# Optimization experiments

Hardware: AMD Instinct MI355X
Metric: run time of the kernel (lower is better)

The kernel has to match this reference:

```python
import jax, jax.numpy as jnp
import numpy as np

H = 256
B = 4096          # number of graphs / motifs in batch
NF = 131072       # focal atoms
NR = 262144       # residues
V = 8001          # vocab.size() + 1
TOPK = 5
DIST_THRESH = 6.0


def setup_inputs() -> dict:
    key = jax.random.key(0)
    ks = jax.random.split(key, 12)
    h_ctx_focal = jax.random.normal(ks[0], (NF, H), dtype=jnp.float32)
    pos_ctx_focal = jax.random.normal(ks[1], (NF, 3), dtype=jnp.float32)
    current_wid = jax.random.randint(ks[2], (B,), 0, V)
    current_atoms_batch = jnp.sort(jax.random.randint(ks[3], (NF,), 0, B))
    h_residue = jax.random.normal(ks[4], (NR, H), dtype=jnp.float32)
    residue_pos = jax.random.normal(ks[5], (NR, 3, 3), dtype=jnp.float32)
    amino_acid_batch = jnp.sort(jax.random.randint(ks[6], (NR,), 0, B))
    emb_weight = jax.random.normal(ks[7], (V, H), dtype=jnp.float32) * 0.02
    mlp_w1 = jax.random.normal(ks[8], (3 * H, H), dtype=jnp.float32) * (1.0 / np.sqrt(3 * H))
    mlp_b1 = jnp.zeros((H,), dtype=jnp.float32)
    mlp_w2 = jax.random.normal(ks[9], (H, H), dtype=jnp.float32) * (1.0 / np.sqrt(H))
    mlp_b2 = jnp.zeros((H,), dtype=jnp.float32)
    return {
        'h_ctx_focal': h_ctx_focal, 'pos_ctx_focal': pos_ctx_focal,
        'current_wid': current_wid, 'current_atoms_batch': current_atoms_batch,
        'h_residue': h_residue, 'residue_pos': residue_pos,
        'amino_acid_batch': amino_acid_batch, 'emb_weight': emb_weight,
        'mlp_w1': mlp_w1, 'mlp_b1': mlp_b1, 'mlp_w2': mlp_w2, 'mlp_b2': mlp_b2,
    }


def reference(h_ctx_focal, pos_ctx_focal, current_wid, current_atoms_batch,
              h_residue, residue_pos, amino_acid_batch,
              emb_weight, mlp_w1, mlp_b1, mlp_w2, mlp_b2):
    nB = current_wid.shape[0]
    # scatter_add over focal atoms -> [B, H]
    node_hiddens = jax.ops.segment_sum(h_ctx_focal, current_atoms_batch, num_segments=nB)
    # embedding lookup -> [B, H]
    motif_hiddens = emb_weight[current_wid]
    # scatter_mean of positions -> [B, 3]
    pos_sum = jax.ops.segment_sum(pos_ctx_focal, current_atoms_batch, num_segments=nB)
    counts = jax.ops.segment_sum(jnp.ones((pos_ctx_focal.shape[0],), jnp.float32),
                                 current_atoms_batch, num_segments=nB)
    center_pos = pos_sum / jnp.maximum(counts, 1.0)[:, None]
    # CA position of each residue, distance mask (< 6 A from motif center)
    ca_pos = residue_pos[:, 1, :]                                  # [NR, 3]
    dist = jnp.linalg.norm(ca_pos - center_pos[amino_acid_batch], axis=1)
    mask = dist < DIST_THRESH                                      # [NR]
    # masked scatter_add of residue embeddings -> [B, H]
    residue_emb = jax.ops.segment_sum(jnp.where(mask[:, None], h_residue, 0.0),
                                      amino_acid_batch, num_segments=nB)
    # motif MLP (2 layers) + projection onto embedding table
    pred_vecs = jnp.concatenate([node_hiddens, motif_hiddens, residue_emb], axis=-1)  # [B, 3H]
    h = jax.nn.relu(pred_vecs @ mlp_w1 + mlp_b1)
    mh = h @ mlp_w2 + mlp_b2                                        # [B, H]
    pred_scores = mh @ emb_weight.T                                 # [B, V]
    # top-k + random selection among top-k
    _, select_pool = jax.lax.top_k(pred_scores, TOPK)               # [B, k]
    idx = jax.random.randint(jax.random.key(1), (nB,), 0, TOPK)
    preds = jnp.take_along_axis(select_pool, idx[:, None], axis=1)[:, 0]
    return (pred_scores, preds)
```

## Files before the change

### kernel.cpp

```cpp
#include <hip/hip_runtime.h>
#include <hip/hip_bf16.h>
#include <cstdint>

#define HD   256
#define BSZ  4096
#define NFV  131072
#define NRV  262144
#define VV   8001
#define TOPKN 5
#define RBOFF (BSZ + 1)
#define EPAD 8064

typedef __attribute__((ext_vector_type(8))) short short8v;
typedef __attribute__((ext_vector_type(4))) float float4v;

__host__ __device__ __forceinline__ unsigned rotl32(unsigned v, int d) {
  return (v << d) | (v >> (32 - d));
}

__host__ __device__ __forceinline__ void threefry2x32(
    unsigned k0, unsigned k1, unsigned x0, unsigned x1,
    unsigned& o0, unsigned& o1) {
  unsigned ks2 = k0 ^ k1 ^ 0x1BD11BDAu;
  x0 += k0; x1 += k1;
  x0 += x1; x1 = rotl32(x1, 13); x1 ^= x0;
  x0 += x1; x1 = rotl32(x1, 15); x1 ^= x0;
  x0 += x1; x1 = rotl32(x1, 26); x1 ^= x0;
  x0 += x1; x1 = rotl32(x1,  6); x1 ^= x0;
  x0 += k1; x1 += ks2 + 1u;
  x0 += x1; x1 = rotl32(x1, 17); x1 ^= x0;
  x0 += x1; x1 = rotl32(x1, 29); x1 ^= x0;
  x0 += x1; x1 = rotl32(x1, 16); x1 ^= x0;
  x0 += x1; x1 = rotl32(x1, 24); x1 ^= x0;
  x0 += ks2; x1 += k0 + 2u;
  x0 += x1; x1 = rotl32(x1, 13); x1 ^= x0;
  x0 += x1; x1 = rotl32(x1, 15); x1 ^= x0;
  x0 += x1; x1 = rotl32(x1, 26); x1 ^= x0;
  x0 += x1; x1 = rotl32(x1,  6); x1 ^= x0;
  x0 += k0; x1 += k1 + 3u;
  x0 += x1; x1 = rotl32(x1, 17); x1 ^= x0;
  x0 += x1; x1 = rotl32(x1, 29); x1 ^= x0;
  x0 += x1; x1 = rotl32(x1, 16); x1 ^= x0;
  x0 += x1; x1 = rotl32(x1, 24); x1 ^= x0;
  x0 += k1; x1 += ks2 + 4u;
  x0 += x1; x1 = rotl32(x1, 13); x1 ^= x0;
  x0 += x1; x1 = rotl32(x1, 15); x1 ^= x0;
  x0 += x1; x1 = rotl32(x1, 26); x1 ^= x0;
  x0 += x1; x1 = rotl32(x1,  6); x1 ^= x0;
  x0 += ks2; x1 += k0 + 5u;
  o0 = x0; o1 = x1;
}

__device__ __forceinline__ unsigned short f2bf(float f) {
  unsigned u = __float_as_uint(f);
  unsigned r = (u + 0x7FFFu + ((u >> 16) & 1u)) >> 16;
  return (unsigned short)r;
}
__device__ __forceinline__ float bf2f(unsigned short s) {
  return __uint_as_float(((unsigned)s) << 16);
}

__device__ __forceinline__ int lower_bound_i(const int* __restrict__ a, int n, int v) {
  int lo = 0, hi = n;
  while (lo < hi) { int m = (lo + hi) >> 1; if (a[m] < v) lo = m + 1; else hi = m; }
  return lo;
}

__device__ __forceinline__ void gl16(const unsigned short* g, unsigned short* l) {
  __builtin_amdgcn_global_load_lds(
      (const __attribute__((address_space(1))) unsigned int*)g,
      (__attribute__((address_space(3))) unsigned int*)l, 16, 0, 0);
}

__global__ __launch_bounds__(256) void prep_kernel(
    const int* __restrict__ ab, const int* __restrict__ rb, int* __restrict__ bounds,
    const float* __restrict__ emb, unsigned short* __restrict__ ehi,
    unsigned short* __restrict__ elo,
    const float* __restrict__ w1, unsigned short* __restrict__ w1th,
    unsigned short* __restrict__ w1tl,
    const float* __restrict__ w2, unsigned short* __restrict__ w2th,
    unsigned short* __restrict__ w2tl) {
  int blk = blockIdx.x, t = threadIdx.x;
  if (blk < 33) {
    int i = blk * 256 + t;
    if (i <= BSZ) bounds[i] = lower_bound_i(ab, NFV, i);
    else if (i <= 2 * BSZ + 1) bounds[i] = lower_bound_i(rb, NRV, i - RBOFF);
  } else if (blk < 33 + 2016) {
    size_t i = ((size_t)(blk - 33) * 256 + t) * 4;
    int row = (int)(i >> 8);
    float f[4] = {0.f, 0.f, 0.f, 0.f};
    if (row < VV) {
      float4 v = *reinterpret_cast<const float4*>(&emb[i]);
      f[0] = v.x; f[1] = v.y; f[2] = v.z; f[3] = v.w;
    }
    unsigned short h[4], l[4];
#pragma unroll
    for (int j = 0; j < 4; ++j) {
      h[j] = f2bf(f[j]);
      l[j] = f2bf(f[j] - bf2f(h[j]));
    }
    *reinterpret_cast<uint2*>(&ehi[i]) = *reinterpret_cast<uint2*>(h);
    *reinterpret_cast<uint2*>(&elo[i]) = *reinterpret_cast<uint2*>(l);
  } else if (blk < 33 + 2016 + 768) {
    int i = (blk - 2049) * 256 + t;
    int n = i / 768, k = i - n * 768;
    float v = w1[k * 256 + n];
    unsigned short h = f2bf(v);
    w1th[i] = h; w1tl[i] = f2bf(v - bf2f(h));
  } else {
    int i = (blk - 2817) * 256 + t;
    int n = i >> 8, k = i & 255;
    float v = w2[k * 256 + n];
    unsigned short h = f2bf(v);
    w2th[i] = h; w2tl[i] = f2bf(v - bf2f(h));
  }
}

__global__ __launch_bounds__(256) void mask_kernel(
    const float* __restrict__ pcf, const float* __restrict__ rpos,
    const int* __restrict__ bounds, unsigned char* __restrict__ mask) {
  int lane = threadIdx.x & 63;
  int b = blockIdx.x * 4 + (threadIdx.x >> 6);
  int a0 = bounds[b], a1 = bounds[b + 1];
  int r0 = bounds[RBOFF + b], r1 = bounds[RBOFF + b + 1];

  float cp = 0.f;
  if (lane < 3 && a0 < a1) {
    float nv = pcf[(size_t)a0 * 3 + lane];
    for (int aa = a0; aa < a1; ++aa) {
      float cv = nv;
      if (aa + 1 < a1) nv = pcf[(size_t)(aa + 1) * 3 + lane];
      cp += cv;
    }
  }
  if (lane < 3) cp = cp / fmaxf((float)(a1 - a0), 1.0f);
  float cx = __shfl(cp, 0), cy = __shfl(cp, 1), cz = __shfl(cp, 2);

  for (int r = r0 + lane; r < r1; r += 64) {
    float dx = rpos[(size_t)r * 9 + 3] - cx;
    float dy = rpos[(size_t)r * 9 + 4] - cy;
    float dz = rpos[(size_t)r * 9 + 5] - cz;
    mask[r] = (dx * dx + dy * dy + dz * dz < 36.0f) ? 1 : 0;
  }
}

__global__ __launch_bounds__(256) void fuse_seg_kernel(
    const float* __restrict__ hcf, const int* __restrict__ wid,
    const float* __restrict__ hres, const unsigned char* __restrict__ mask,
    const unsigned short* __restrict__ ehi, const unsigned short* __restrict__ elo,
    const int* __restrict__ bounds,
    unsigned short* __restrict__ pvh, unsigned short* __restrict__ pvl) {
  int t = threadIdx.x;
  int lane = t & 63, wv = t >> 6;
  int half = wv & 1;
  int b = blockIdx.x * 2 + (wv >> 1);
  int a0 = bounds[b], a1 = bounds[b + 1];
  int r0 = bounds[RBOFF + b], r1 = bounds[RBOFF + b + 1];
  size_t off = (size_t)lane * 4;
  size_t o = (size_t)b * 768;

  __shared__ float4v part[4][64];

  float4v acc = 0.f;
  for (int c = half;; c += 2) {
    int base = a0 + 8 * c;
    if (base >= a1) break;
    if (base + 8 <= a1) {
      float4v v[8];
#pragma unroll
      for (int j = 0; j < 8; ++j)
        v[j] = *reinterpret_cast<const float4v*>(&hcf[(size_t)(base + j) * HD + off]);
      acc += ((v[0] + v[1]) + (v[2] + v[3])) + ((v[4] + v[5]) + (v[6] + v[7]));
    } else {
      for (int a = base; a < a1; ++a)
        acc += *reinterpret_cast<const float4v*>(&hcf[(size_t)a * HD + off]);
    }
  }
  part[wv][lane] = acc;
  __syncthreads();
  if (half == 0) {
    float4v s = part[wv][lane] + part[wv + 1][lane];
    unsigned short h[4], l[4];
#pragma unroll
    for (int j = 0; j < 4; ++j) {
      h[j] = f2bf(s[j]); l[j] = f2bf(s[j] - bf2f(h[j]));
    }
    *reinterpret_cast<uint2*>(&pvh[o + off]) = *reinterpret_cast<uint2*>(h);
    *reinterpret_cast<uint2*>(&pvl[o + off]) = *reinterpret_cast<uint2*>(l);
  } else {
    *reinterpret_cast<uint2*>(&pvh[o + 256 + off]) =
        *reinterpret_cast<const uint2*>(&ehi[(size_t)wid[b] * 256 + off]);
    *reinterpret_cast<uint2*>(&pvl[o + 256 + off]) =
        *reinterpret_cast<const uint2*>(&elo[(size_t)wid[b] * 256 + off]);
  }
  __syncthreads();

  float4v racc = 0.f;
  int ra = (r0 + 7) & ~7;
  if (half == 0) {
    int pe = ra < r1 ? ra : r1;
    for (int r = r0; r < pe; ++r) {
      float4v v = *reinterpret_cast<const float4v*>(&hres[(size_t)r * HD + off]);
      if (mask[r]) racc += v;
    }
  }
  for (int c = half;; c += 2) {
    int base = ra + 8 * c;
    if (base >= r1) break;
    if (base + 8 <= r1) {
      uint2 mw = *reinterpret_cast<const uint2*>(&mask[base]);
      float4v v[8];
#pragma unroll
      for (int j = 0; j < 8; ++j)
        v[j] = *reinterpret_cast<const float4v*>(&hres[(size_t)(base + j) * HD + off]);
      float4v s0 = 0.f, s1 = 0.f, s2 = 0.f, s3 = 0.f;
      if (mw.x & 0x000000FFu) s0 += v[0];
      if (mw.x & 0x0000FF00u) s1 += v[1];
      if (mw.x & 0x00FF0000u) s2 += v[2];
      if (mw.x & 0xFF000000u) s3 += v[3];
      if (mw.y & 0x000000FFu) s0 += v[4];
      if (mw.y & 0x0000FF00u) s1 += v[5];
      if (mw.y & 0x00FF0000u) s2 += v[6];
      if (mw.y & 0xFF000000u) s3 += v[7];
      racc += (s0 + s1) + (s2 + s3);
    } else {
      for (int r = base; r < r1; ++r) {
        float4v v = *reinterpret_cast<const float4v*>(&hres[(size_t)r * HD + off]);
        if (mask[r]) racc += v;
      }
    }
  }
  part[wv][lane] = racc;
  __syncthreads();
  if (half == 0) {
    float4v s = part[wv][lane] + part[wv + 1][lane];
    unsigned short h[4], l[4];
#pragma unroll
    for (int j = 0; j < 4; ++j) {
      h[j] = f2bf(s[j]); l[j] = f2bf(s[j] - bf2f(h[j]));
    }
    *reinterpret_cast<uint2*>(&pvh[o + 512 + off]) = *reinterpret_cast<uint2*>(h);
    *reinterpret_cast<uint2*>(&pvl[o + 512 + off]) = *reinterpret_cast<uint2*>(l);
  }
}

template <bool RELU, int K, int N>
__global__ __launch_bounds__(256) void mlp_gemm_kernel(
    const unsigned short* __restrict__ Ahg, const unsigned short* __restrict__ Alg,
    const unsigned short* __restrict__ Bhg, const unsigned short* __restrict__ Blg,
    const float* __restrict__ bias,
    unsigned short* __restrict__ Chi, unsigned short* __restrict__ Clo) {
  __shared__ __attribute__((aligned(16))) unsigned short Ahs[64][72];
  __shared__ __attribute__((aligned(16))) unsigned short Als[64][72];
  __shared__ __attribute__((aligned(16))) unsigned short Bhs[64][72];
  __shared__ __attribute__((aligned(16))) unsigned short Bls[64][72];

  int t = threadIdx.x;
  int bm = blockIdx.y * 64, bn = blockIdx.x * 64;
  int lane = t & 63, wv = t >> 6;
  int wm = wv >> 1, wn = wv & 1;
  int lr = lane & 15, lg = lane >> 4;
  float4v acc[2][2] = {};

  int srow = t >> 2, sc = (t & 3) * 16;

  for (int kb = 0; kb < K; kb += 64) {
    size_t ga = (size_t)(bm + srow) * K + kb + sc;
    size_t gb = (size_t)(bn + srow) * K + kb + sc;
    *reinterpret_cast<short8v*>(&Ahs[srow][sc]) = *reinterpret_cast<const short8v*>(&Ahg[ga]);
    *reinterpret_cast<short8v*>(&Ahs[srow][sc + 8]) = *reinterpret_cast<const short8v*>(&Ahg[ga + 8]);
    *reinterpret_cast<short8v*>(&Als[srow][sc]) = *reinterpret_cast<const short8v*>(&Alg[ga]);
    *reinterpret_cast<short8v*>(&Als[srow][sc + 8]) = *reinterpret_cast<const short8v*>(&Alg[ga + 8]);
    *reinterpret_cast<short8v*>(&Bhs[srow][sc]) = *reinterpret_cast<const short8v*>(&Bhg[gb]);
    *reinterpret_cast<short8v*>(&Bhs[srow][sc + 8]) = *reinterpret_cast<const short8v*>(&Bhg[gb + 8]);
    *reinterpret_cast<short8v*>(&Bls[srow][sc]) = *reinterpret_cast<const short8v*>(&Blg[gb]);
    *reinterpret_cast<short8v*>(&Bls[srow][sc + 8]) = *reinterpret_cast<const short8v*>(&Blg[gb + 8]);
    __syncthreads();

#pragma unroll
    for (int ks = 0; ks < 2; ++ks) {
      int ko = ks * 32 + lg * 8;
      short8v aH[2], aL[2], bH[2], bL[2];
#pragma unroll
      for (int f = 0; f < 2; ++f) {
        aH[f] = *reinterpret_cast<const short8v*>(&Ahs[wm * 32 + f * 16 + lr][ko]);
        aL[f] = *reinterpret_cast<const short8v*>(&Als[wm * 32 + f * 16 + lr][ko]);
        bH[f] = *reinterpret_cast<const short8v*>(&Bhs[wn * 32 + f * 16 + lr][ko]);
        bL[f] = *reinterpret_cast<const short8v*>(&Bls[wn * 32 + f * 16 + lr][ko]);
      }
#pragma unroll
      for (int mf = 0; mf < 2; ++mf)
#pragma unroll
        for (int nf = 0; nf < 2; ++nf) {
          acc[mf][nf] = __builtin_amdgcn_mfma_f32_16x16x32_bf16(
              aH[mf], bH[nf], acc[mf][nf], 0, 0, 0);
          acc[mf][nf] = __builtin_amdgcn_mfma_f32_16x16x32_bf16(
              aH[mf], bL[nf], acc[mf][nf], 0, 0, 0);
          acc[mf][nf] = __builtin_amdgcn_mfma_f32_16x16x32_bf16(
              aL[mf], bH[nf], acc[mf][nf], 0, 0, 0);
        }
    }
    __syncthreads();
  }

#pragma unroll
  for (int mf = 0; mf < 2; ++mf)
#pragma unroll
    for (int nf = 0; nf < 2; ++nf) {
      int col = bn + wn * 32 + nf * 16 + lr;
      float bv = bias[col];
#pragma unroll
      for (int rr = 0; rr < 4; ++rr) {
        int row = bm + wm * 32 + mf * 16 + lg * 4 + rr;
        float v = acc[mf][nf][rr] + bv;
        if (RELU) v = fmaxf(v, 0.f);
        unsigned short h = f2bf(v);
        Chi[(size_t)row * N + col] = h;
        Clo[(size_t)row * N + col] = f2bf(v - bf2f(h));
      }
    }
}

__global__ __launch_bounds__(256, 2) void score_gemm_kernel(
    const unsigned short* __restrict__ Ahg, const unsigned short* __restrict__ Alg,
    const unsigned short* __restrict__ Bhg, const unsigned short* __restrict__ Blg,
    float* __restrict__ C) {
  __shared__ __attribute__((aligned(16))) unsigned short Ah[128 * 64];
  __shared__ __attribute__((aligned(16))) unsigned short Al[128 * 64];
  __shared__ __attribute__((aligned(16))) unsigned short Bh[128 * 64];
  __shared__ __attribute__((aligned(16))) unsigned short Bl[128 * 64];

  int t = threadIdx.x;
  int bm = blockIdx.x * 128;
  int bn = blockIdx.y * 128;
  int lane = t & 63, wv = t >> 6;
  int wm = wv >> 1, wn = wv & 1;
  int lr = lane & 15, lg = lane >> 4;

  float4v acc[4][4] = {};

  int rsub = lane >> 3;
  int cb = (lane & 7) * 16;

  for (int kb = 0; kb < 256; kb += 64) {
#pragma unroll
    for (int j = 0; j < 4; ++j) {
      int ch = wv * 4 + j;
      int grow = ch * 8 + rsub;
      int scb = cb ^ ((grow & 7) << 4);
      size_t goA = (size_t)(bm + grow) * 256 + kb + (scb >> 1);
      size_t goB = (size_t)(bn + grow) * 256 + kb + (scb >> 1);
      unsigned lo = ch * 512 + lane * 8;
      gl16(&Ahg[goA], &Ah[lo]);
      gl16(&Alg[goA], &Al[lo]);
      gl16(&Bhg[goB], &Bh[lo]);
      gl16(&Blg[goB], &Bl[lo]);
    }
    __syncthreads();

#pragma unroll
    for (int ks = 0; ks < 2; ++ks) {
      int bo = (ks * 32 + lg * 8) * 2;
      short8v aH[4], aL[4], bH[4], bL[4];
#pragma unroll
      for (int f = 0; f < 4; ++f) {
        int ra = wm * 64 + f * 16 + lr;
        int rb2 = wn * 64 + f * 16 + lr;
        int oa = ra * 128 + (bo ^ ((ra & 7) << 4));
        int ob2 = rb2 * 128 + (bo ^ ((rb2 & 7) << 4));
        aH[f] = *reinterpret_cast<const short8v*>((const char*)Ah + oa);
        aL[f] = *reinterpret_cast<const short8v*>((const char*)Al + oa);
        bH[f] = *reinterpret_cast<const short8v*>((const char*)Bh + ob2);
        bL[f] = *reinterpret_cast<const short8v*>((const char*)Bl + ob2);
      }
#pragma unroll
      for (int mf = 0; mf < 4; ++mf)
#pragma unroll
        for (int nf = 0; nf < 4; ++nf) {
          acc[mf][nf] = __builtin_amdgcn_mfma_f32_16x16x32_bf16(
              aH[mf], bH[nf], acc[mf][nf], 0, 0, 0);
          acc[mf][nf] = __builtin_amdgcn_mfma_f32_16x16x32_bf16(
              aH[mf], bL[nf], acc[mf][nf], 0, 0, 0);
          acc[mf][nf] = __builtin_amdgcn_mfma_f32_16x16x32_bf16(
              aL[mf], bH[nf], acc[mf][nf], 0, 0, 0);
        }
    }
    __syncthreads();
  }

#pragma unroll
  for (int mf = 0; mf < 4; ++mf)
#pragma unroll
    for (int nf = 0; nf < 4; ++nf) {
      int col = bn + wn * 64 + nf * 16 + lr;
      if (col < VV) {
#pragma unroll
        for (int rr = 0; rr < 4; ++rr) {
          int row = bm + wm * 64 + mf * 16 + lg * 4 + rr;
          C[(size_t)row * VV + col] = acc[mf][nf][rr];
        }
      }
    }
}

#define BETTER(av, ai, bv, bi) ((av) > (bv) || ((av) == (bv) && (ai) < (bi)))

__global__ __launch_bounds__(256) void topk_kernel(
    const float* __restrict__ scores, float* __restrict__ preds,
    unsigned k1a, unsigned k1b, unsigned k2a, unsigned k2b) {
  int lane = threadIdx.x & 63;
  int row = (blockIdx.x << 2) + (threadIdx.x >> 6);
  const float* s = scores + (size_t)row * VV;

  const float NEG = -__builtin_huge_valf();
  float v0 = NEG, v1 = NEG, v2 = NEG, v3 = NEG, v4 = NEG;
  int i0 = 0x7FFFFFFF, i1 = 0x7FFFFFFF, i2 = 0x7FFFFFFF, i3 = 0x7FFFFFFF, i4 = 0x7FFFFFFF;

  for (int v = lane; v < VV; v += 64) {
    float val = s[v];
    if (BETTER(val, v, v4, i4)) {
      if (BETTER(val, v, v3, i3)) {
        v4 = v3; i4 = i3;
        if (BETTER(val, v, v2, i2)) {
          v3 = v2; i3 = i2;
          if (BETTER(val, v, v1, i1)) {
            v2 = v1; i2 = i1;
            if (BETTER(val, v, v0, i0)) {
              v1 = v0; i1 = i0; v0 = val; i0 = v;
            } else { v1 = val; i1 = v; }
          } else { v2 = val; i2 = v; }
        } else { v3 = val; i3 = v; }
      } else { v4 = val; i4 = v; }
    }
  }

  int sel0, sel1, sel2, sel3, sel4;
#pragma unroll
  for (int p = 0; p < TOPKN; ++p) {
    float bv = v0; int bi = i0;
#pragma unroll
    for (int off = 32; off > 0; off >>= 1) {
      float ov = __shfl_xor(bv, off);
      int   oi = __shfl_xor(bi, off);
      if (BETTER(ov, oi, bv, bi)) { bv = ov; bi = oi; }
    }
    if (p == 0) sel0 = bi; else if (p == 1) sel1 = bi; else if (p == 2) sel2 = bi;
    else if (p == 3) sel3 = bi; else sel4 = bi;
    if (bi == i0) {
      v0 = v1; i0 = i1; v1 = v2; i1 = i2; v2 = v3; i2 = i3; v3 = v4; i3 = i4;
      v4 = NEG; i4 = 0x7FFFFFFF;
    }
  }

  if (lane == 0) {
    unsigned i = (unsigned)row;
    unsigned h0, h1, l0, l1;
    threefry2x32(k1a, k1b, 0u, i, h0, h1);
    threefry2x32(k2a, k2b, 0u, i, l0, l1);
    unsigned idx = (((h0 ^ h1) % 5u) + ((l0 ^ l1) % 5u)) % 5u;
    int pick = (idx == 0) ? sel0 : (idx == 1) ? sel1 : (idx == 2) ? sel2
             : (idx == 3) ? sel3 : sel4;
    preds[row] = (float)pick;
  }
}

extern "C" void kernel_launch(void* const* d_in, const int* in_sizes, int n_in,
                              void* d_out, int out_size, void* d_ws, size_t ws_size,
                              hipStream_t stream) {
  const float* hcf  = (const float*)d_in[0];
  const float* pcf  = (const float*)d_in[1];
  const int*   wid  = (const int*)d_in[2];
  const int*   ab   = (const int*)d_in[3];
  const float* hres = (const float*)d_in[4];
  const float* rpos = (const float*)d_in[5];
  const int*   rb   = (const int*)d_in[6];
  const float* emb  = (const float*)d_in[7];
  const float* w1   = (const float*)d_in[8];
  const float* bb1  = (const float*)d_in[9];
  const float* w2   = (const float*)d_in[10];
  const float* bb2  = (const float*)d_in[11];

  float* out    = (float*)d_out;
  float* scores = out;
  float* preds  = out + (size_t)BSZ * VV;

  char* ob = (char*)d_out;
  unsigned short* pvh  = (unsigned short*)(ob);
  unsigned short* pvl  = (unsigned short*)(ob + 0x600000);
  unsigned short* hh   = (unsigned short*)(ob + 0xC00000);
  unsigned short* hl   = (unsigned short*)(ob + 0xE00000);
  unsigned short* w1th = (unsigned short*)(ob + 0x1000000);
  unsigned short* w1tl = (unsigned short*)(ob + 0x1060000);
  unsigned short* w2th = (unsigned short*)(ob + 0x10C0000);
  unsigned short* w2tl = (unsigned short*)(ob + 0x10E0000);

  char* ws = (char*)d_ws;
  int*            bounds = (int*)(ws);
  unsigned char*  mask   = (unsigned char*)(ws + 0x10000);
  unsigned short* mh_hi  = (unsigned short*)(ws + 0x100000);
  unsigned short* mh_lo  = (unsigned short*)(ws + 0x300000);
  unsigned short* emb_hi = (unsigned short*)(ws + 0x500000);
  unsigned short* emb_lo = (unsigned short*)(ws + 0x900000);

  prep_kernel<<<33 + 2016 + 768 + 256, 256, 0, stream>>>(
      ab, rb, bounds, emb, emb_hi, emb_lo, w1, w1th, w1tl, w2, w2th, w2tl);

  mask_kernel<<<BSZ / 4, 256, 0, stream>>>(pcf, rpos, bounds, mask);

  fuse_seg_kernel<<<BSZ / 2, 256, 0, stream>>>(
      hcf, wid, hres, mask, emb_hi, emb_lo, bounds, pvh, pvl);

  mlp_gemm_kernel<true, 768, 256><<<dim3(4, 64), 256, 0, stream>>>(
      pvh, pvl, w1th, w1tl, bb1, hh, hl);
  mlp_gemm_kernel<false, 256, 256><<<dim3(4, 64), 256, 0, stream>>>(
      hh, hl, w2th, w2tl, bb2, mh_hi, mh_lo);

  score_gemm_kernel<<<dim3(BSZ / 128, EPAD / 128), 256, 0, stream>>>(
      mh_hi, mh_lo, emb_hi, emb_lo, scores);

  unsigned k1a, k1b, k2a, k2b;
  threefry2x32(0u, 1u, 0u, 0u, k1a, k1b);
  threefry2x32(0u, 1u, 0u, 1u, k2a, k2b);
  topk_kernel<<<BSZ / 4, 256, 0, stream>>>(scores, preds, k1a, k1b, k2a, k2b);
}
```

Baseline: 291.4 us.

## Double-buffer score GEMM LDS tiles with K-step 32 and prefetch

The score GEMM now uses two LDS buffers with a K tile of 32 instead of a single buffer with a K tile of 64. The next tile's global-to-LDS loads are issued before the current tile's MFMAs, so load latency can overlap compute. This also removes one barrier per iteration. The swizzle changes to fit 64-byte rows. The cost is twice as many loop iterations with fewer MFMAs each, and one barrier per step remains.

```diff
diff --git a/kernel.cpp b/kernel.cpp
--- a/kernel.cpp
+++ b/kernel.cpp
@@ -321,14 +321,16 @@
     }
 }
 
+#define SWZB(row) ((((row) >> 1) & 3) << 4)
+
 __global__ __launch_bounds__(256, 2) void score_gemm_kernel(
     const unsigned short* __restrict__ Ahg, const unsigned short* __restrict__ Alg,
     const unsigned short* __restrict__ Bhg, const unsigned short* __restrict__ Blg,
     float* __restrict__ C) {
-  __shared__ __attribute__((aligned(16))) unsigned short Ah[128 * 64];
-  __shared__ __attribute__((aligned(16))) unsigned short Al[128 * 64];
-  __shared__ __attribute__((aligned(16))) unsigned short Bh[128 * 64];
-  __shared__ __attribute__((aligned(16))) unsigned short Bl[128 * 64];
+  __shared__ __attribute__((aligned(16))) unsigned short Ah[2 * 4096];
+  __shared__ __attribute__((aligned(16))) unsigned short Al[2 * 4096];
+  __shared__ __attribute__((aligned(16))) unsigned short Bh[2 * 4096];
+  __shared__ __attribute__((aligned(16))) unsigned short Bl[2 * 4096];
 
   int t = threadIdx.x;
   int bm = blockIdx.x * 128;
@@ -339,53 +341,62 @@
 
   float4v acc[4][4] = {};
 
-  int rsub = lane >> 3;
-  int cb = (lane & 7) * 16;
-
-  for (int kb = 0; kb < 256; kb += 64) {
-#pragma unroll
-    for (int j = 0; j < 4; ++j) {
-      int ch = wv * 4 + j;
-      int grow = ch * 8 + rsub;
-      int scb = cb ^ ((grow & 7) << 4);
-      size_t goA = (size_t)(bm + grow) * 256 + kb + (scb >> 1);
-      size_t goB = (size_t)(bn + grow) * 256 + kb + (scb >> 1);
-      unsigned lo = ch * 512 + lane * 8;
-      gl16(&Ahg[goA], &Ah[lo]);
-      gl16(&Alg[goA], &Al[lo]);
-      gl16(&Bhg[goB], &Bh[lo]);
-      gl16(&Blg[goB], &Bl[lo]);
-    }
-    __syncthreads();
-
-#pragma unroll
-    for (int ks = 0; ks < 2; ++ks) {
-      int bo = (ks * 32 + lg * 8) * 2;
-      short8v aH[4], aL[4], bH[4], bL[4];
-#pragma unroll
-      for (int f = 0; f < 4; ++f) {
-        int ra = wm * 64 + f * 16 + lr;
-        int rb2 = wn * 64 + f * 16 + lr;
-        int oa = ra * 128 + (bo ^ ((ra & 7) << 4));
-        int ob2 = rb2 * 128 + (bo ^ ((rb2 & 7) << 4));
-        aH[f] = *reinterpret_cast<const short8v*>((const char*)Ah + oa);
-        aL[f] = *reinterpret_cast<const short8v*>((const char*)Al + oa);
-        bH[f] = *reinterpret_cast<const short8v*>((const char*)Bh + ob2);
-        bL[f] = *reinterpret_cast<const short8v*>((const char*)Bl + ob2);
+  int sidx0 = (wv * 2 + 0) * 512 + lane * 8;
+  int sidx1 = (wv * 2 + 1) * 512 + lane * 8;
+  int srow0 = sidx0 >> 5, srow1 = sidx1 >> 5;
+  int scb0 = ((sidx0 & 31) * 2) ^ SWZB(srow0);
+  int scb1 = ((sidx1 & 31) * 2) ^ SWZB(srow1);
+
+  auto stage = [&](int kt, int bufb) {
+    unsigned base = bufb * 4096;
+    size_t gA0 = (size_t)(bm + srow0) * 256 + kt * 32 + (scb0 >> 1);
+    size_t gB0 = (size_t)(bn + srow0) * 256 + kt * 32 + (scb0 >> 1);
+    size_t gA1 = (size_t)(bm + srow1) * 256 + kt * 32 + (scb1 >> 1);
+    size_t gB1 = (size_t)(bn + srow1) * 256 + kt * 32 + (scb1 >> 1);
+    gl16(&Ahg[gA0], &Ah[base + sidx0]);
+    gl16(&Alg[gA0], &Al[base + sidx0]);
+    gl16(&Bhg[gB0], &Bh[base + sidx0]);
+    gl16(&Blg[gB0], &Bl[base + sidx0]);
+    gl16(&Ahg[gA1], &Ah[base + sidx1]);
+    gl16(&Alg[gA1], &Al[base + sidx1]);
+    gl16(&Bhg[gB1], &Bh[base + sidx1]);
+    gl16(&Blg[gB1], &Bl[base + sidx1]);
+  };
+
+  stage(0, 0);
+  __syncthreads();
+
+  int bo = lg * 16;
+  for (int kt = 0; kt < 8; ++kt) {
+    int cur = kt & 1;
+    if (kt < 7) stage(kt + 1, cur ^ 1);
+
+    unsigned cbase = cur * 8192;
+    short8v aH[4], aL[4], bH[4], bL[4];
+#pragma unroll
+    for (int f = 0; f < 4; ++f) {
+      int rA = wm * 64 + f * 16 + lr;
+      int rB = wn * 64 + f * 16 + lr;
+      unsigned oa = cbase + rA * 64 + (bo ^ SWZB(rA));
+      unsigned ob = cbase + rB * 64 + (bo ^ SWZB(rB));
+      aH[f] = *reinterpret_cast<const short8v*>((const char*)Ah + oa);
+      aL[f] = *reinterpret_cast<const short8v*>((const char*)Al + oa);
+      bH[f] = *reinterpret_cast<const short8v*>((const char*)Bh + ob);
+      bL[f] = *reinterpret_cast<const short8v*>((const char*)Bl + ob);
+    }
+#pragma unroll
+    for (int mf = 0; mf < 4; ++mf)
+#pragma unroll
+      for (int nf = 0; nf < 4; ++nf) {
+        acc[mf][nf] = __builtin_amdgcn_mfma_f32_16x16x32_bf16(
+            aH[mf], bH[nf], acc[mf][nf], 0, 0, 0);
+        acc[mf][nf] = __builtin_amdgcn_mfma_f32_16x16x32_bf16(
+            aH[mf], bL[nf], acc[mf][nf], 0, 0, 0);
+        acc[mf][nf] = __builtin_amdgcn_mfma_f32_16x16x32_bf16(
+            aL[mf], bH[nf], acc[mf][nf], 0, 0, 0);
       }
-#pragma unroll
-      for (int mf = 0; mf < 4; ++mf)
-#pragma unroll
-        for (int nf = 0; nf < 4; ++nf) {
-          acc[mf][nf] = __builtin_amdgcn_mfma_f32_16x16x32_bf16(
-              aH[mf], bH[nf], acc[mf][nf], 0, 0, 0);
-          acc[mf][nf] = __builtin_amdgcn_mfma_f32_16x16x32_bf16(
-              aH[mf], bL[nf], acc[mf][nf], 0, 0, 0);
-          acc[mf][nf] = __builtin_amdgcn_mfma_f32_16x16x32_bf16(
-              aL[mf], bH[nf], acc[mf][nf], 0, 0, 0);
-        }
-    }
-    __syncthreads();
+
+    if (kt < 7) __syncthreads();
   }
 
 #pragma unroll
```

After: 304.5 us. 4.5% more time.

## Pack bf16 hi/lo split into concatenated K=768 operands for score GEMM

Applied to the files above, without the earlier changes.

Instead of keeping separate hi and lo bf16 arrays and issuing three MFMAs per fragment pair, the embedding table is stored as [hi|lo|hi] and the MLP output as [hi|hi|lo] rows of width 768. A single K=768 GEMM then computes hH*eH + hH*eL + hL*eH. This halves the LDS footprint and the number of separate load streams, which allows three blocks per CU. In exchange it writes and reads a 3x-wide duplicated operand and runs a longer K loop.

```diff
diff --git a/kernel.cpp b/kernel.cpp
--- a/kernel.cpp
+++ b/kernel.cpp
@@ -74,8 +74,7 @@
 
 __global__ __launch_bounds__(256) void prep_kernel(
     const int* __restrict__ ab, const int* __restrict__ rb, int* __restrict__ bounds,
-    const float* __restrict__ emb, unsigned short* __restrict__ ehi,
-    unsigned short* __restrict__ elo,
+    const float* __restrict__ emb, unsigned short* __restrict__ e3,
     const float* __restrict__ w1, unsigned short* __restrict__ w1th,
     unsigned short* __restrict__ w1tl,
     const float* __restrict__ w2, unsigned short* __restrict__ w2th,
@@ -87,7 +86,7 @@
     else if (i <= 2 * BSZ + 1) bounds[i] = lower_bound_i(rb, NRV, i - RBOFF);
   } else if (blk < 33 + 2016) {
     size_t i = ((size_t)(blk - 33) * 256 + t) * 4;
-    int row = (int)(i >> 8);
+    int row = (int)(i >> 8), k = (int)(i & 255);
     float f[4] = {0.f, 0.f, 0.f, 0.f};
     if (row < VV) {
       float4 v = *reinterpret_cast<const float4*>(&emb[i]);
@@ -99,8 +98,10 @@
       h[j] = f2bf(f[j]);
       l[j] = f2bf(f[j] - bf2f(h[j]));
     }
-    *reinterpret_cast<uint2*>(&ehi[i]) = *reinterpret_cast<uint2*>(h);
-    *reinterpret_cast<uint2*>(&elo[i]) = *reinterpret_cast<uint2*>(l);
+    size_t base = (size_t)row * 768 + k;
+    *reinterpret_cast<uint2*>(&e3[base])       = *reinterpret_cast<uint2*>(h);
+    *reinterpret_cast<uint2*>(&e3[base + 256]) = *reinterpret_cast<uint2*>(l);
+    *reinterpret_cast<uint2*>(&e3[base + 512]) = *reinterpret_cast<uint2*>(h);
   } else if (blk < 33 + 2016 + 768) {
     int i = (blk - 2049) * 256 + t;
     int n = i / 768, k = i - n * 768;
@@ -147,8 +148,7 @@
 __global__ __launch_bounds__(256) void fuse_seg_kernel(
     const float* __restrict__ hcf, const int* __restrict__ wid,
     const float* __restrict__ hres, const unsigned char* __restrict__ mask,
-    const unsigned short* __restrict__ ehi, const unsigned short* __restrict__ elo,
-    const int* __restrict__ bounds,
+    const unsigned short* __restrict__ e3, const int* __restrict__ bounds,
     unsigned short* __restrict__ pvh, unsigned short* __restrict__ pvl) {
   int t = threadIdx.x;
   int lane = t & 63, wv = t >> 6;
@@ -189,9 +189,9 @@
     *reinterpret_cast<uint2*>(&pvl[o + off]) = *reinterpret_cast<uint2*>(l);
   } else {
     *reinterpret_cast<uint2*>(&pvh[o + 256 + off]) =
-        *reinterpret_cast<const uint2*>(&ehi[(size_t)wid[b] * 256 + off]);
+        *reinterpret_cast<const uint2*>(&e3[(size_t)wid[b] * 768 + off]);
     *reinterpret_cast<uint2*>(&pvl[o + 256 + off]) =
-        *reinterpret_cast<const uint2*>(&elo[(size_t)wid[b] * 256 + off]);
+        *reinterpret_cast<const uint2*>(&e3[(size_t)wid[b] * 768 + 256 + off]);
   }
   __syncthreads();
 
@@ -244,7 +244,7 @@
   }
 }
 
-template <bool RELU, int K, int N>
+template <bool RELU, int K, int N, bool CONCAT>
 __global__ __launch_bounds__(256) void mlp_gemm_kernel(
     const unsigned short* __restrict__ Ahg, const unsigned short* __restrict__ Alg,
     const unsigned short* __restrict__ Bhg, const unsigned short* __restrict__ Blg,
@@ -315,20 +315,23 @@
         float v = acc[mf][nf][rr] + bv;
         if (RELU) v = fmaxf(v, 0.f);
         unsigned short h = f2bf(v);
-        Chi[(size_t)row * N + col] = h;
-        Clo[(size_t)row * N + col] = f2bf(v - bf2f(h));
+        unsigned short l = f2bf(v - bf2f(h));
+        if (CONCAT) {
+          size_t base = (size_t)row * 768 + col;
+          Chi[base] = h; Chi[base + 256] = h; Chi[base + 512] = l;
+        } else {
+          Chi[(size_t)row * N + col] = h;
+          Clo[(size_t)row * N + col] = l;
+        }
       }
     }
 }
 
-__global__ __launch_bounds__(256, 2) void score_gemm_kernel(
-    const unsigned short* __restrict__ Ahg, const unsigned short* __restrict__ Alg,
-    const unsigned short* __restrict__ Bhg, const unsigned short* __restrict__ Blg,
+__global__ __launch_bounds__(256, 3) void score_gemm_kernel(
+    const unsigned short* __restrict__ A3, const unsigned short* __restrict__ B3,
     float* __restrict__ C) {
-  __shared__ __attribute__((aligned(16))) unsigned short Ah[128 * 64];
-  __shared__ __attribute__((aligned(16))) unsigned short Al[128 * 64];
-  __shared__ __attribute__((aligned(16))) unsigned short Bh[128 * 64];
-  __shared__ __attribute__((aligned(16))) unsigned short Bl[128 * 64];
+  __shared__ __attribute__((aligned(16))) unsigned short As[128 * 64];
+  __shared__ __attribute__((aligned(16))) unsigned short Bs[128 * 64];
 
   int t = threadIdx.x;
   int bm = blockIdx.x * 128;
@@ -342,48 +345,39 @@
   int rsub = lane >> 3;
   int cb = (lane & 7) * 16;
 
-  for (int kb = 0; kb < 256; kb += 64) {
+  for (int kb = 0; kb < 768; kb += 64) {
 #pragma unroll
     for (int j = 0; j < 4; ++j) {
       int ch = wv * 4 + j;
       int grow = ch * 8 + rsub;
       int scb = cb ^ ((grow & 7) << 4);
-      size_t goA = (size_t)(bm + grow) * 256 + kb + (scb >> 1);
-      size_t goB = (size_t)(bn + grow) * 256 + kb + (scb >> 1);
+      size_t goA = (size_t)(bm + grow) * 768 + kb + (scb >> 1);
+      size_t goB = (size_t)(bn + grow) * 768 + kb + (scb >> 1);
       unsigned lo = ch * 512 + lane * 8;
-      gl16(&Ahg[goA], &Ah[lo]);
-      gl16(&Alg[goA], &Al[lo]);
-      gl16(&Bhg[goB], &Bh[lo]);
-      gl16(&Blg[goB], &Bl[lo]);
+      gl16(&A3[goA], &As[lo]);
+      gl16(&B3[goB], &Bs[lo]);
     }
     __syncthreads();
 
 #pragma unroll
     for (int ks = 0; ks < 2; ++ks) {
       int bo = (ks * 32 + lg * 8) * 2;
-      short8v aH[4], aL[4], bH[4], bL[4];
+      short8v aF[4], bF[4];
 #pragma unroll
       for (int f = 0; f < 4; ++f) {
-        int ra = wm * 64 + f * 16 + lr;
-        int rb2 = wn * 64 + f * 16 + lr;
-        int oa = ra * 128 + (bo ^ ((ra & 7) << 4));
-        int ob2 = rb2 * 128 + (bo ^ ((rb2 & 7) << 4));
-        aH[f] = *reinterpret_cast<const short8v*>((const char*)Ah + oa);
-        aL[f] = *reinterpret_cast<const short8v*>((const char*)Al + oa);
-        bH[f] = *reinterpret_cast<const short8v*>((const char*)Bh + ob2);
-        bL[f] = *reinterpret_cast<const short8v*>((const char*)Bl + ob2);
+        int rA = wm * 64 + f * 16 + lr;
+        int rB = wn * 64 + f * 16 + lr;
+        aF[f] = *reinterpret_cast<const short8v*>(
+            (const char*)As + rA * 128 + (bo ^ ((rA & 7) << 4)));
+        bF[f] = *reinterpret_cast<const short8v*>(
+            (const char*)Bs + rB * 128 + (bo ^ ((rB & 7) << 4)));
       }
 #pragma unroll
       for (int mf = 0; mf < 4; ++mf)
 #pragma unroll
-        for (int nf = 0; nf < 4; ++nf) {
+        for (int nf = 0; nf < 4; ++nf)
           acc[mf][nf] = __builtin_amdgcn_mfma_f32_16x16x32_bf16(
-              aH[mf], bH[nf], acc[mf][nf], 0, 0, 0);
-          acc[mf][nf] = __builtin_amdgcn_mfma_f32_16x16x32_bf16(
-              aH[mf], bL[nf], acc[mf][nf], 0, 0, 0);
-          acc[mf][nf] = __builtin_amdgcn_mfma_f32_16x16x32_bf16(
-              aL[mf], bH[nf], acc[mf][nf], 0, 0, 0);
-        }
+              aF[mf], bF[nf], acc[mf][nf], 0, 0, 0);
     }
     __syncthreads();
   }
@@ -497,26 +491,23 @@
   char* ws = (char*)d_ws;
   int*            bounds = (int*)(ws);
   unsigned char*  mask   = (unsigned char*)(ws + 0x10000);
-  unsigned short* mh_hi  = (unsigned short*)(ws + 0x100000);
-  unsigned short* mh_lo  = (unsigned short*)(ws + 0x300000);
-  unsigned short* emb_hi = (unsigned short*)(ws + 0x500000);
-  unsigned short* emb_lo = (unsigned short*)(ws + 0x900000);
+  unsigned short* mh3    = (unsigned short*)(ws + 0x100000);
+  unsigned short* e3     = (unsigned short*)(ws + 0x700000);
 
   prep_kernel<<<33 + 2016 + 768 + 256, 256, 0, stream>>>(
-      ab, rb, bounds, emb, emb_hi, emb_lo, w1, w1th, w1tl, w2, w2th, w2tl);
+      ab, rb, bounds, emb, e3, w1, w1th, w1tl, w2, w2th, w2tl);
 
   mask_kernel<<<BSZ / 4, 256, 0, stream>>>(pcf, rpos, bounds, mask);
 
   fuse_seg_kernel<<<BSZ / 2, 256, 0, stream>>>(
-      hcf, wid, hres, mask, emb_hi, emb_lo, bounds, pvh, pvl);
-
-  mlp_gemm_kernel<true, 768, 256><<<dim3(4, 64), 256, 0, stream>>>(
+      hcf, wid, hres, mask, e3, bounds, pvh, pvl);
+
+  mlp_gemm_kernel<true, 768, 256, false><<<dim3(4, 64), 256, 0, stream>>>(
       pvh, pvl, w1th, w1tl, bb1, hh, hl);
-  mlp_gemm_kernel<false, 256, 256><<<dim3(4, 64), 256, 0, stream>>>(
-      hh, hl, w2th, w2tl, bb2, mh_hi, mh_lo);
-
-  score_gemm_kernel<<<dim3(BSZ / 128, EPAD / 128), 256, 0, stream>>>(
-      mh_hi, mh_lo, emb_hi, emb_lo, scores);
+  mlp_gemm_kernel<false, 256, 256, true><<<dim3(4, 64), 256, 0, stream>>>(
+      hh, hl, w2th, w2tl, bb2, mh3, nullptr);
+
+  score_gemm_kernel<<<dim3(BSZ / 128, EPAD / 128), 256, 0, stream>>>(mh3, e3, scores);
 
   unsigned k1a, k1b, k2a, k2b;
   threefry2x32(0u, 1u, 0u, 0u, k1a, k1b);
```

New measurement: 296.8 us. About the same (+1.9%).
